# Optimization experiments

Hardware: AMD Instinct MI355X
Metric: run time of the kernel (lower is better)

## Reference

```python
import jax, jax.numpy as jnp
import numpy as np

N_NODES = 50000
N_EDGES = 800000
IN_FEAT = 256
OUT_FEAT = 128
P_EDGE = 0.2   # edge dropout rate
P_NODE = 0.1   # node-feature dropout rate
BN_EPS = 1e-5


def setup_inputs() -> dict:
    key = jax.random.key(0)
    ks = jax.random.split(key, 8)
    features = jax.random.normal(ks[0], (N_NODES, IN_FEAT), dtype=jnp.float32)
    W = jax.random.normal(ks[1], (IN_FEAT, OUT_FEAT), dtype=jnp.float32) / np.sqrt(IN_FEAT)
    b = jnp.zeros((OUT_FEAT,), dtype=jnp.float32)
    gamma = jnp.ones((OUT_FEAT,), dtype=jnp.float32)
    beta = jnp.zeros((OUT_FEAT,), dtype=jnp.float32)
    src = jax.random.randint(ks[2], (N_EDGES,), 0, N_NODES, dtype=jnp.int64)
    dst = jax.random.randint(ks[3], (N_EDGES,), 0, N_NODES, dtype=jnp.int64)
    edge_rand = jax.random.uniform(ks[4], (N_EDGES,), dtype=jnp.float32)
    node_rand = jax.random.uniform(ks[5], (N_NODES, OUT_FEAT), dtype=jnp.float32)
    return {"features": features, "W": W, "b": b, "gamma": gamma, "beta": beta,
            "src": src, "dst": dst, "edge_rand": edge_rand, "node_rand": node_rand}


def reference(features, W, b, gamma, beta, src, dst, edge_rand, node_rand):
    dt = features.dtype
    # --- edge dropout: keep-mask over edges (no rescale, per DropEdge convention) ---
    emask = (edge_rand >= P_EDGE).astype(dt)                      # [E]
    # --- GCN conv, norm='both' on the dropped graph ---
    h = features @ W                                              # [N, out] (W first: out < in)
    deg_src = jax.ops.segment_sum(emask, src, num_segments=N_NODES)  # out-degrees
    deg_dst = jax.ops.segment_sum(emask, dst, num_segments=N_NODES)  # in-degrees
    coef = emask * jax.lax.rsqrt(jnp.maximum(deg_src[src], 1.0) * jnp.maximum(deg_dst[dst], 1.0))
    msg = h[src] * coef[:, None]                                  # [E, out]
    agg = jax.ops.segment_sum(msg, dst, num_segments=N_NODES) + b  # [N, out]
    # --- BatchNorm1d (training mode: batch statistics over nodes) ---
    mean = jnp.mean(agg, axis=0)
    var = jnp.var(agg, axis=0)
    y = (agg - mean) * jax.lax.rsqrt(var + BN_EPS) * gamma + beta
    # --- node-feature dropout (inverted scaling) ---
    nmask = (node_rand >= P_NODE).astype(dt) / (1.0 - P_NODE)
    return y * nmask
```

## Files before the change

kernel.cpp:

```cpp
#include <hip/hip_runtime.h>

#define N_NODES 50000
#define N_EDGES 800000
#define IN_FEAT 256
#define OUT_FEAT 128
#define P_EDGE 0.2f
#define P_NODE 0.1f
#define BN_EPS 1e-5f
#define NPART 8
#define CAP_Q 24
#define PART_STRIDE 1200000
#define GEMM_BLOCKS 782
#define EDGE_BLOCKS 782
#define ZERO_BLOCKS 782
#define PREPW_BLOCKS 128
#define MERGE_BLOCKS 196
#define AGG_BLOCKS 1024
#define FIN_BLOCKS 8

typedef __bf16 bf16x8 __attribute__((ext_vector_type(8)));
typedef float floatx4 __attribute__((ext_vector_type(4)));
typedef float f32x4 __attribute__((ext_vector_type(4)));
typedef int i32x4 __attribute__((ext_vector_type(4)));

__device__ inline float bflo(unsigned u) { return __uint_as_float(u << 16); }
__device__ inline float bfhi(unsigned u) { return __uint_as_float(u & 0xffff0000u); }

__global__ __launch_bounds__(256) void k_init(const float* __restrict__ W,
    uint4* __restrict__ zero_base, __bf16* __restrict__ Wt) {
  if (blockIdx.x < ZERO_BLOCKS) {
    int i = blockIdx.x * 256 + threadIdx.x;
    if (i < 200000) zero_base[i] = make_uint4(0u, 0u, 0u, 0u);
  } else {
    int idx = (blockIdx.x - ZERO_BLOCKS) * 256 + threadIdx.x;
    int k = idx >> 7, n = idx & 127;
    Wt[n * IN_FEAT + k] = (__bf16)W[idx];
  }
}

__device__ inline bf16x8 cvt8(f32x4 a, f32x4 b) {
  bf16x8 v;
  v[0] = (__bf16)a[0]; v[1] = (__bf16)a[1]; v[2] = (__bf16)a[2]; v[3] = (__bf16)a[3];
  v[4] = (__bf16)b[0]; v[5] = (__bf16)b[1]; v[6] = (__bf16)b[2]; v[7] = (__bf16)b[3];
  return v;
}

__global__ __launch_bounds__(256) void k_edge(
    const int* __restrict__ src, const int* __restrict__ dst,
    const float* __restrict__ er, unsigned* __restrict__ deg_src_q,
    unsigned* __restrict__ deg_dst_q, unsigned short* __restrict__ parts) {
  const int q = blockIdx.x & 7;
  unsigned* dsq = deg_src_q + q * N_NODES;
  unsigned* ddq = deg_dst_q + q * N_NODES;
  unsigned short* pq = parts + (size_t)q * PART_STRIDE;
  int t = blockIdx.x * 256 + threadIdx.x;
  if (t < N_EDGES / 4) {
    f32x4 e4 = ((const f32x4*)er)[t];
    i32x4 s4 = ((const i32x4*)src)[t];
    i32x4 d4 = ((const i32x4*)dst)[t];
    const bool k0 = e4[0] >= P_EDGE, k1 = e4[1] >= P_EDGE;
    const bool k2 = e4[2] >= P_EDGE, k3 = e4[3] >= P_EDGE;
    unsigned p0 = 0xffffffffu, p1 = 0xffffffffu, p2 = 0xffffffffu, p3 = 0xffffffffu;
    if (k0) p0 = atomicAdd(&ddq[d4[0]], 1u);
    if (k1) p1 = atomicAdd(&ddq[d4[1]], 1u);
    if (k2) p2 = atomicAdd(&ddq[d4[2]], 1u);
    if (k3) p3 = atomicAdd(&ddq[d4[3]], 1u);
    if (k0) atomicAdd(&dsq[s4[0]], 1u);
    if (k1) atomicAdd(&dsq[s4[1]], 1u);
    if (k2) atomicAdd(&dsq[s4[2]], 1u);
    if (k3) atomicAdd(&dsq[s4[3]], 1u);
    if (p0 < CAP_Q) pq[(unsigned)d4[0] * CAP_Q + p0] = (unsigned short)s4[0];
    if (p1 < CAP_Q) pq[(unsigned)d4[1] * CAP_Q + p1] = (unsigned short)s4[1];
    if (p2 < CAP_Q) pq[(unsigned)d4[2] * CAP_Q + p2] = (unsigned short)s4[2];
    if (p3 < CAP_Q) pq[(unsigned)d4[3] * CAP_Q + p3] = (unsigned short)s4[3];
  }
}

__global__ __launch_bounds__(256) void k_merge(const unsigned* __restrict__ deg_src_q,
    const unsigned* __restrict__ deg_dst_q, unsigned long long* __restrict__ cnt8,
    unsigned char* __restrict__ tot8, unsigned char* __restrict__ deg_src_m) {
  int n = blockIdx.x * 256 + threadIdx.x;
  if (n < N_NODES) {
    unsigned ts = 0;
#pragma unroll
    for (int q = 0; q < NPART; q++) ts += deg_src_q[q * N_NODES + n];
    deg_src_m[n] = (unsigned char)(ts > 255u ? 255u : ts);
    unsigned long long pack = 0;
    unsigned tt = 0;
#pragma unroll
    for (int q = 0; q < NPART; q++) {
      unsigned c = deg_dst_q[q * N_NODES + n];
      tt += c;
      c = c > CAP_Q ? CAP_Q : c;
      pack |= (unsigned long long)c << (8 * q);
    }
    cnt8[n] = pack;
    tot8[n] = (unsigned char)(tt > 255u ? 255u : tt);
  }
}

__global__ __launch_bounds__(256, 2) void k_gemm(const float* __restrict__ feat,
    const __bf16* __restrict__ Wt, __bf16* __restrict__ h) {
  __shared__ char lds[65536];
  const int t = threadIdx.x;

  const uint4* wsrc = (const uint4*)Wt;
#pragma unroll
  for (int i = 0; i < 16; i++) {
    int c = i * 256 + t;
    unsigned o = (unsigned)c * 16u;
    unsigned row = o >> 9;
    *(uint4*)(lds + (o ^ ((row & 7u) << 4))) = wsrc[c];
  }
  __syncthreads();

  const int lane = t & 63;
  const int wave = t >> 6;
  const int l16 = lane & 15;
  const int quad = lane >> 4;
  const int m0 = blockIdx.x * 64 + wave * 16;

  int mload = m0 + l16;
  if (mload >= N_NODES) mload = N_NODES - 1;

  bf16x8 a[8];
#pragma unroll
  for (int kk = 0; kk < 8; kk++) {
    const f32x4* p = (const f32x4*)(feat + (size_t)mload * IN_FEAT + kk * 32 + quad * 8);
    a[kk] = cvt8(p[0], p[1]);
  }

  floatx4 acc[8];
#pragma unroll
  for (int g = 0; g < 8; g++) {
    const unsigned row = (unsigned)(g * 16 + l16);
    const unsigned base = row * 512u + (unsigned)quad * 16u;
    const unsigned swz = (row & 7u) << 4;
    floatx4 c = {0.f, 0.f, 0.f, 0.f};
#pragma unroll
    for (int kk = 0; kk < 8; kk++) {
      bf16x8 b = *(const bf16x8*)(lds + ((base + (unsigned)kk * 64u) ^ swz));
      c = __builtin_amdgcn_mfma_f32_16x16x32_bf16(a[kk], b, c, 0, 0, 0);
    }
    acc[g] = c;
  }
  __syncthreads();

  char* hb = lds + wave * 16384;
#pragma unroll
  for (int g = 0; g < 8; g++) {
#pragma unroll
    for (int r = 0; r < 4; r++) {
      unsigned row = (unsigned)(quad * 4 + r);
      unsigned o = row * 256u + (unsigned)(g * 16 + l16) * 2u;
      *(__bf16*)(hb + (o ^ ((row & 7u) << 4))) = (__bf16)acc[g][r];
    }
  }
#pragma unroll
  for (int j = 0; j < 4; j++) {
    unsigned row = (unsigned)(lane >> 4) + (unsigned)j * 4u;
    unsigned o = row * 256u + (unsigned)(lane & 15) * 16u;
    uint4 v = *(const uint4*)(hb + (o ^ ((row & 7u) << 4)));
    int grow = m0 + (int)row;
    if (grow < N_NODES)
      *(uint4*)((char*)h + (size_t)grow * 256 + (size_t)(lane & 15) * 16) = v;
  }
}

__global__ __launch_bounds__(256) void k_agg(const unsigned short* __restrict__ h,
    const unsigned short* __restrict__ parts, const unsigned char* __restrict__ deg_src_m,
    const unsigned long long* __restrict__ cnt8, const unsigned char* __restrict__ tot8,
    const float* __restrict__ bias, float* __restrict__ out,
    float* __restrict__ psum, float* __restrict__ pssq) {
  const int wid = threadIdx.x >> 6;
  const int lane = threadIdx.x & 63;
  const int g = lane >> 4;
  const int cl = lane & 15;
  const int wave_global = blockIdx.x * 4 + wid;

  float b8[8];
#pragma unroll
  for (int j = 0; j < 8; j++) b8[j] = bias[cl * 8 + j];

  float s8[8], ss8[8];
#pragma unroll
  for (int j = 0; j < 8; j++) { s8[j] = 0.f; ss8[j] = 0.f; }

  for (int d = wave_global; d < N_NODES; d += AGG_BLOCKS * 4) {
    const unsigned long long c8 = cnt8[d];
    unsigned P[8];
    unsigned run = 0;
#pragma unroll
    for (int q = 0; q < 8; q++) { P[q] = run; run += (unsigned)((c8 >> (8 * q)) & 0xffull); }
    const unsigned lim = run;
    const unsigned dbase = (unsigned)d * CAP_Q;

    float acc[8];
#pragma unroll
    for (int j = 0; j < 8; j++) acc[j] = 0.f;

#pragma unroll 2
    for (unsigned i = 0; i < lim; i += 4) {
      unsigned e = i + (unsigned)g;
      bool valid = e < lim;
      unsigned ec = valid ? e : 0u;
      unsigned qq = 0, off = 0;
#pragma unroll
      for (int j = 1; j < 8; j++) {
        bool ge = ec >= P[j];
        qq += ge ? 1u : 0u;
        off = ge ? P[j] : off;
      }
      unsigned idx = (unsigned)parts[(size_t)qq * PART_STRIDE + dbase + (ec - off)];
      unsigned dg = deg_src_m[idx];
      float r = valid ? rsqrtf((float)(dg ? dg : 1u)) : 0.f;
      uint4 u = *(const uint4*)(h + (size_t)idx * OUT_FEAT + cl * 8);
      acc[0] = fmaf(bflo(u.x), r, acc[0]);
      acc[1] = fmaf(bfhi(u.x), r, acc[1]);
      acc[2] = fmaf(bflo(u.y), r, acc[2]);
      acc[3] = fmaf(bfhi(u.y), r, acc[3]);
      acc[4] = fmaf(bflo(u.z), r, acc[4]);
      acc[5] = fmaf(bfhi(u.z), r, acc[5]);
      acc[6] = fmaf(bflo(u.w), r, acc[6]);
      acc[7] = fmaf(bfhi(u.w), r, acc[7]);
    }
#pragma unroll
    for (int j = 0; j < 8; j++) {
      acc[j] += __shfl_xor(acc[j], 16);
      acc[j] += __shfl_xor(acc[j], 32);
    }
    if (g == 0) {
      unsigned tot = tot8[d];
      float sc = rsqrtf((float)(tot ? tot : 1u));
      float o[8];
#pragma unroll
      for (int j = 0; j < 8; j++) {
        o[j] = fmaf(acc[j], sc, b8[j]);
        s8[j] += o[j];
        ss8[j] = fmaf(o[j], o[j], ss8[j]);
      }
      float4 o0 = make_float4(o[0], o[1], o[2], o[3]);
      float4 o1 = make_float4(o[4], o[5], o[6], o[7]);
      *(float4*)(out + (size_t)d * OUT_FEAT + cl * 8) = o0;
      *(float4*)(out + (size_t)d * OUT_FEAT + cl * 8 + 4) = o1;
    }
  }

  __shared__ float ls[4][16][8], lss[4][16][8];
  if (g == 0) {
#pragma unroll
    for (int j = 0; j < 8; j++) { ls[wid][cl][j] = s8[j]; lss[wid][cl][j] = ss8[j]; }
  }
  __syncthreads();
  if (threadIdx.x < 128) {
    int pcl = threadIdx.x >> 3, pj = threadIdx.x & 7;
    float t = ls[0][pcl][pj] + ls[1][pcl][pj] + ls[2][pcl][pj] + ls[3][pcl][pj];
    float t2 = lss[0][pcl][pj] + lss[1][pcl][pj] + lss[2][pcl][pj] + lss[3][pcl][pj];
    psum[blockIdx.x * OUT_FEAT + threadIdx.x] = t;
    pssq[blockIdx.x * OUT_FEAT + threadIdx.x] = t2;
  }
}

__global__ __launch_bounds__(256) void k_fin(const float* __restrict__ psum,
    const float* __restrict__ pssq, const float* __restrict__ gamma,
    const float* __restrict__ beta, float* __restrict__ a_coef,
    float* __restrict__ b_coef) {
  const int col16 = threadIdx.x & 15;
  const int slice = threadIdx.x >> 4;
  const int c = blockIdx.x * 16 + col16;
  float t = 0.f, t2 = 0.f;
  for (int b = slice; b < AGG_BLOCKS; b += 16) {
    t += psum[b * OUT_FEAT + c];
    t2 += pssq[b * OUT_FEAT + c];
  }
  __shared__ float S[16][17], S2[16][17];
  S[slice][col16] = t;
  S2[slice][col16] = t2;
  __syncthreads();
  if (threadIdx.x < 16) {
    float ts = 0.f, tss = 0.f;
#pragma unroll
    for (int s = 0; s < 16; s++) { ts += S[s][threadIdx.x]; tss += S2[s][threadIdx.x]; }
    int cc = blockIdx.x * 16 + threadIdx.x;
    float mean = ts * (1.0f / N_NODES);
    float var = tss * (1.0f / N_NODES) - mean * mean;
    float a = gamma[cc] * rsqrtf(var + BN_EPS);
    a_coef[cc] = a;
    b_coef[cc] = fmaf(-mean, a, beta[cc]);
  }
}

__global__ __launch_bounds__(256) void k_norm(float* __restrict__ out,
    const float* __restrict__ node_rand, const float* __restrict__ a_coef,
    const float* __restrict__ b_coef) {
  const size_t total4 = (size_t)N_NODES * OUT_FEAT / 4;
  size_t i = (size_t)blockIdx.x * 256 + threadIdx.x;
  if (i < total4) {
    int c0 = (int)((i * 4) & 127);
    f32x4 v = ((const f32x4*)out)[i];
    f32x4 nr = ((const f32x4*)node_rand)[i];
    f32x4 a = *(const f32x4*)(a_coef + c0);
    f32x4 b = *(const f32x4*)(b_coef + c0);
    const float inv = 1.0f / (1.0f - P_NODE);
    f32x4 o;
    o[0] = (nr[0] >= P_NODE ? inv : 0.f) * fmaf(v[0], a[0], b[0]);
    o[1] = (nr[1] >= P_NODE ? inv : 0.f) * fmaf(v[1], a[1], b[1]);
    o[2] = (nr[2] >= P_NODE ? inv : 0.f) * fmaf(v[2], a[2], b[2]);
    o[3] = (nr[3] >= P_NODE ? inv : 0.f) * fmaf(v[3], a[3], b[3]);
    ((f32x4*)out)[i] = o;
  }
}

extern "C" void kernel_launch(void* const* d_in, const int* in_sizes, int n_in,
                              void* d_out, int out_size, void* d_ws, size_t ws_size,
                              hipStream_t stream) {
  const float* feat  = (const float*)d_in[0];
  const float* W     = (const float*)d_in[1];
  const float* bias  = (const float*)d_in[2];
  const float* gamma = (const float*)d_in[3];
  const float* beta  = (const float*)d_in[4];
  const int*   src   = (const int*)d_in[5];
  const int*   dst   = (const int*)d_in[6];
  const float* er    = (const float*)d_in[7];
  const float* nr    = (const float*)d_in[8];
  float* out = (float*)d_out;

  char* ws = (char*)d_ws;
  __bf16*             h         = (__bf16*)            (ws + 0);
  unsigned short*     parts     = (unsigned short*)    (ws + 12800000);
  __bf16*             Wt        = (__bf16*)            (ws + 32000000);
  unsigned*           deg_src_q = (unsigned*)          (ws + 32065536);
  unsigned*           deg_dst_q = (unsigned*)          (ws + 33665536);
  unsigned long long* cnt8      = (unsigned long long*)(ws + 35265536);
  unsigned char*      tot8      = (unsigned char*)     (ws + 35665536);
  unsigned char*      deg_src_m = (unsigned char*)     (ws + 35715584);
  float*              psum      = (float*)             (ws + 35765760);
  float*              pssq      = (float*)             (ws + 36290048);
  float*              a_coef    = (float*)             (ws + 36814336);
  float*              b_coef    = (float*)             (ws + 36814848);

  k_init<<<ZERO_BLOCKS + PREPW_BLOCKS, 256, 0, stream>>>(
      W, (uint4*)(ws + 32065536), Wt);
  k_edge<<<EDGE_BLOCKS, 256, 0, stream>>>(src, dst, er, deg_src_q, deg_dst_q, parts);
  k_gemm<<<GEMM_BLOCKS, 256, 0, stream>>>(feat, Wt, h);
  k_merge<<<MERGE_BLOCKS, 256, 0, stream>>>(deg_src_q, deg_dst_q, cnt8, tot8, deg_src_m);
  k_agg<<<AGG_BLOCKS, 256, 0, stream>>>((const unsigned short*)h, parts,
      deg_src_m, cnt8, tot8, bias, out, psum, pssq);
  k_fin<<<FIN_BLOCKS, 256, 0, stream>>>(psum, pssq, gamma, beta, a_coef, b_coef);
  k_norm<<<(N_NODES * OUT_FEAT / 4 + 255) / 256, 256, 0, stream>>>(out, nr, a_coef, b_coef);
}
```

Before: 287.0 us.

## Fuse edge and GEMM kernels, compact partitions into per-node buckets in merge

Merges the edge-count/scatter kernel and the GEMM into one launch, alternating groups of eight blocks so the atomic-heavy edge work and the compute-bound GEMM run concurrently. The merge kernel now copies each node's eight partition slices into one contiguous bucket of up to 64 sources and packs count and total degree into a single 16-bit word. This removes the per-edge partition search in the aggregation loop. Per-partition capacity drops from 24 to 16 and aggregation blocks double. The fused kernel's launch bounds no longer allow two blocks per SM, which may lower GEMM occupancy. The serial per-thread bucket copy in merge adds work.

```diff
diff --git a/kernel.cpp b/kernel.cpp
--- a/kernel.cpp
+++ b/kernel.cpp
@@ -8,14 +8,16 @@
 #define P_NODE 0.1f
 #define BN_EPS 1e-5f
 #define NPART 8
-#define CAP_Q 24
-#define PART_STRIDE 1200000
+#define CAP_Q 16
+#define PART_STRIDE 800000
+#define CAP 64
 #define GEMM_BLOCKS 782
 #define EDGE_BLOCKS 782
+#define EG_BLOCKS 1568
 #define ZERO_BLOCKS 782
 #define PREPW_BLOCKS 128
 #define MERGE_BLOCKS 196
-#define AGG_BLOCKS 1024
+#define AGG_BLOCKS 2048
 #define FIN_BLOCKS 8
 
 typedef __bf16 bf16x8 __attribute__((ext_vector_type(8)));
@@ -45,15 +47,14 @@
   return v;
 }
 
-__global__ __launch_bounds__(256) void k_edge(
+__device__ void edge_body(int ebid, int q,
     const int* __restrict__ src, const int* __restrict__ dst,
     const float* __restrict__ er, unsigned* __restrict__ deg_src_q,
     unsigned* __restrict__ deg_dst_q, unsigned short* __restrict__ parts) {
-  const int q = blockIdx.x & 7;
   unsigned* dsq = deg_src_q + q * N_NODES;
   unsigned* ddq = deg_dst_q + q * N_NODES;
   unsigned short* pq = parts + (size_t)q * PART_STRIDE;
-  int t = blockIdx.x * 256 + threadIdx.x;
+  int t = ebid * 256 + threadIdx.x;
   if (t < N_EDGES / 4) {
     f32x4 e4 = ((const f32x4*)er)[t];
     i32x4 s4 = ((const i32x4*)src)[t];
@@ -76,30 +77,7 @@
   }
 }
 
-__global__ __launch_bounds__(256) void k_merge(const unsigned* __restrict__ deg_src_q,
-    const unsigned* __restrict__ deg_dst_q, unsigned long long* __restrict__ cnt8,
-    unsigned char* __restrict__ tot8, unsigned char* __restrict__ deg_src_m) {
-  int n = blockIdx.x * 256 + threadIdx.x;
-  if (n < N_NODES) {
-    unsigned ts = 0;
-#pragma unroll
-    for (int q = 0; q < NPART; q++) ts += deg_src_q[q * N_NODES + n];
-    deg_src_m[n] = (unsigned char)(ts > 255u ? 255u : ts);
-    unsigned long long pack = 0;
-    unsigned tt = 0;
-#pragma unroll
-    for (int q = 0; q < NPART; q++) {
-      unsigned c = deg_dst_q[q * N_NODES + n];
-      tt += c;
-      c = c > CAP_Q ? CAP_Q : c;
-      pack |= (unsigned long long)c << (8 * q);
-    }
-    cnt8[n] = pack;
-    tot8[n] = (unsigned char)(tt > 255u ? 255u : tt);
-  }
-}
-
-__global__ __launch_bounds__(256, 2) void k_gemm(const float* __restrict__ feat,
+__device__ void gemm_body(int bid, const float* __restrict__ feat,
     const __bf16* __restrict__ Wt, __bf16* __restrict__ h) {
   __shared__ char lds[65536];
   const int t = threadIdx.x;
@@ -118,7 +96,7 @@
   const int wave = t >> 6;
   const int l16 = lane & 15;
   const int quad = lane >> 4;
-  const int m0 = blockIdx.x * 64 + wave * 16;
+  const int m0 = bid * 64 + wave * 16;
 
   int mload = m0 + l16;
   if (mload >= N_NODES) mload = N_NODES - 1;
@@ -167,11 +145,52 @@
   }
 }
 
+__global__ __launch_bounds__(256) void k_eg(const float* __restrict__ feat,
+    const __bf16* __restrict__ Wt, __bf16* __restrict__ h,
+    const int* __restrict__ src, const int* __restrict__ dst,
+    const float* __restrict__ er, unsigned* __restrict__ deg_src_q,
+    unsigned* __restrict__ deg_dst_q, unsigned short* __restrict__ parts) {
+  const int bid = blockIdx.x;
+  const int grp = bid >> 3;
+  const int l8 = bid & 7;
+  const int id = (grp >> 1) * 8 + l8;
+  if ((grp & 1) == 0) {
+    if (id < EDGE_BLOCKS) edge_body(id, l8, src, dst, er, deg_src_q, deg_dst_q, parts);
+  } else {
+    if (id < GEMM_BLOCKS) gemm_body(id, feat, Wt, h);
+  }
+}
+
+__global__ __launch_bounds__(256) void k_merge(const unsigned* __restrict__ deg_src_q,
+    const unsigned* __restrict__ deg_dst_q, const unsigned short* __restrict__ parts,
+    unsigned short* __restrict__ bucket, unsigned short* __restrict__ ct,
+    unsigned char* __restrict__ deg_src_m) {
+  int n = blockIdx.x * 256 + threadIdx.x;
+  if (n >= N_NODES) return;
+  unsigned ts = 0;
+#pragma unroll
+  for (int q = 0; q < NPART; q++) ts += deg_src_q[q * N_NODES + n];
+  deg_src_m[n] = (unsigned char)(ts > 255u ? 255u : ts);
+  unsigned short* bo = bucket + (size_t)n * CAP;
+  unsigned w = 0, tt = 0;
+#pragma unroll
+  for (int q = 0; q < NPART; q++) {
+    unsigned c = deg_dst_q[q * N_NODES + n];
+    tt += c;
+    c = c > CAP_Q ? CAP_Q : c;
+    const unsigned short* pq = parts + (size_t)q * PART_STRIDE + (unsigned)n * CAP_Q;
+    for (unsigned i = 0; i < c; i++) {
+      if (w < CAP) bo[w++] = pq[i];
+    }
+  }
+  tt = tt > 255u ? 255u : tt;
+  ct[n] = (unsigned short)(w | (tt << 8));
+}
+
 __global__ __launch_bounds__(256) void k_agg(const unsigned short* __restrict__ h,
-    const unsigned short* __restrict__ parts, const unsigned char* __restrict__ deg_src_m,
-    const unsigned long long* __restrict__ cnt8, const unsigned char* __restrict__ tot8,
-    const float* __restrict__ bias, float* __restrict__ out,
-    float* __restrict__ psum, float* __restrict__ pssq) {
+    const unsigned short* __restrict__ bucket, const unsigned char* __restrict__ deg_src_m,
+    const unsigned short* __restrict__ ct, const float* __restrict__ bias,
+    float* __restrict__ out, float* __restrict__ psum, float* __restrict__ pssq) {
   const int wid = threadIdx.x >> 6;
   const int lane = threadIdx.x & 63;
   const int g = lane >> 4;
@@ -187,14 +206,10 @@
   for (int j = 0; j < 8; j++) { s8[j] = 0.f; ss8[j] = 0.f; }
 
   for (int d = wave_global; d < N_NODES; d += AGG_BLOCKS * 4) {
-    const unsigned long long c8 = cnt8[d];
-    unsigned P[8];
-    unsigned run = 0;
-#pragma unroll
-    for (int q = 0; q < 8; q++) { P[q] = run; run += (unsigned)((c8 >> (8 * q)) & 0xffull); }
-    const unsigned lim = run;
-    const unsigned dbase = (unsigned)d * CAP_Q;
-
+    const unsigned c2 = ct[d];
+    const unsigned lim = c2 & 0xffu;
+    const unsigned tot = c2 >> 8;
+    const unsigned base = (unsigned)d * CAP;
     float acc[8];
 #pragma unroll
     for (int j = 0; j < 8; j++) acc[j] = 0.f;
@@ -203,15 +218,7 @@
     for (unsigned i = 0; i < lim; i += 4) {
       unsigned e = i + (unsigned)g;
       bool valid = e < lim;
-      unsigned ec = valid ? e : 0u;
-      unsigned qq = 0, off = 0;
-#pragma unroll
-      for (int j = 1; j < 8; j++) {
-        bool ge = ec >= P[j];
-        qq += ge ? 1u : 0u;
-        off = ge ? P[j] : off;
-      }
-      unsigned idx = (unsigned)parts[(size_t)qq * PART_STRIDE + dbase + (ec - off)];
+      unsigned idx = (unsigned)bucket[base + (valid ? e : 0u)];
       unsigned dg = deg_src_m[idx];
       float r = valid ? rsqrtf((float)(dg ? dg : 1u)) : 0.f;
       uint4 u = *(const uint4*)(h + (size_t)idx * OUT_FEAT + cl * 8);
@@ -230,7 +237,6 @@
       acc[j] += __shfl_xor(acc[j], 32);
     }
     if (g == 0) {
-      unsigned tot = tot8[d];
       float sc = rsqrtf((float)(tot ? tot : 1u));
       float o[8];
 #pragma unroll
@@ -326,26 +332,27 @@
   float* out = (float*)d_out;
 
   char* ws = (char*)d_ws;
-  __bf16*             h         = (__bf16*)            (ws + 0);
-  unsigned short*     parts     = (unsigned short*)    (ws + 12800000);
-  __bf16*             Wt        = (__bf16*)            (ws + 32000000);
-  unsigned*           deg_src_q = (unsigned*)          (ws + 32065536);
-  unsigned*           deg_dst_q = (unsigned*)          (ws + 33665536);
-  unsigned long long* cnt8      = (unsigned long long*)(ws + 35265536);
-  unsigned char*      tot8      = (unsigned char*)     (ws + 35665536);
-  unsigned char*      deg_src_m = (unsigned char*)     (ws + 35715584);
-  float*              psum      = (float*)             (ws + 35765760);
-  float*              pssq      = (float*)             (ws + 36290048);
-  float*              a_coef    = (float*)             (ws + 36814336);
-  float*              b_coef    = (float*)             (ws + 36814848);
+  __bf16*         h         = (__bf16*)        (ws + 0);
+  unsigned short* parts     = (unsigned short*)(ws + 12800000);
+  float*          psum      = (float*)         (ws + 12800000);
+  float*          pssq      = (float*)         (ws + 13848576);
+  unsigned short* bucket    = (unsigned short*)(ws + 25600000);
+  __bf16*         Wt        = (__bf16*)        (ws + 32000000);
+  unsigned*       deg_src_q = (unsigned*)      (ws + 32065536);
+  unsigned*       deg_dst_q = (unsigned*)      (ws + 33665536);
+  unsigned short* ct        = (unsigned short*)(ws + 35265536);
+  unsigned char*  deg_src_m = (unsigned char*) (ws + 35365632);
+  float*          a_coef    = (float*)         (ws + 35415808);
+  float*          b_coef    = (float*)         (ws + 35416320);
 
   k_init<<<ZERO_BLOCKS + PREPW_BLOCKS, 256, 0, stream>>>(
       W, (uint4*)(ws + 32065536), Wt);
-  k_edge<<<EDGE_BLOCKS, 256, 0, stream>>>(src, dst, er, deg_src_q, deg_dst_q, parts);
-  k_gemm<<<GEMM_BLOCKS, 256, 0, stream>>>(feat, Wt, h);
-  k_merge<<<MERGE_BLOCKS, 256, 0, stream>>>(deg_src_q, deg_dst_q, cnt8, tot8, deg_src_m);
-  k_agg<<<AGG_BLOCKS, 256, 0, stream>>>((const unsigned short*)h, parts,
-      deg_src_m, cnt8, tot8, bias, out, psum, pssq);
+  k_eg<<<EG_BLOCKS, 256, 0, stream>>>(feat, Wt, h, src, dst, er,
+      deg_src_q, deg_dst_q, parts);
+  k_merge<<<MERGE_BLOCKS, 256, 0, stream>>>(deg_src_q, deg_dst_q, parts,
+      bucket, ct, deg_src_m);
+  k_agg<<<AGG_BLOCKS, 256, 0, stream>>>((const unsigned short*)h, bucket,
+      deg_src_m, ct, bias, out, psum, pssq);
   k_fin<<<FIN_BLOCKS, 256, 0, stream>>>(psum, pssq, gamma, beta, a_coef, b_coef);
   k_norm<<<(N_NODES * OUT_FEAT / 4 + 255) / 256, 256, 0, stream>>>(out, nr, a_coef, b_coef);
 }
```

Result: no change. 286.6 us (-0.1%).
